# Kernel tuning notes

Measured on AMD Instinct MI355X. Metric: run time of the kernel, lower is better.

The kernel has to match this reference:

```python
import jax, jax.numpy as jnp
import numpy as np

D_MODEL = 768
D_STATE = 16
K_CONV = 4
BATCH = 2
SEQ = 2048


def setup_inputs() -> dict:
    key = jax.random.key(0)
    ks = jax.random.split(key, 16)
    dm, ds, K = D_MODEL, D_STATE, K_CONV
    s = 0.02
    inp = {
        "x": jax.random.normal(ks[0], (BATCH, SEQ, dm), dtype=jnp.float32),
        # linear weights stored (in, out); y = x @ W + b (equivalent to torch Linear)
        "Wi": jax.random.normal(ks[1], (dm, 2 * dm), dtype=jnp.float32) * s,
        "bi": jnp.zeros((2 * dm,), jnp.float32),
        "Wconv": jax.random.normal(ks[2], (dm, K), dtype=jnp.float32) * s,
        "bconv": jnp.zeros((dm,), jnp.float32),
        "Wdt": jax.random.normal(ks[3], (dm, dm), dtype=jnp.float32) * s,
        "bdt": jnp.zeros((dm,), jnp.float32),
        "WB": jax.random.normal(ks[4], (dm, dm * ds), dtype=jnp.float32) * s,
        "bB": jnp.zeros((dm * ds,), jnp.float32),
        "WC": jax.random.normal(ks[5], (dm, dm * ds), dtype=jnp.float32) * s,
        "bC": jnp.zeros((dm * ds,), jnp.float32),
        "A_log": jnp.zeros((dm, ds), jnp.float32),  # matches nn.Parameter(torch.zeros)
        "D": jnp.ones((dm,), jnp.float32),          # matches nn.Parameter(torch.ones)
        "Wo": jax.random.normal(ks[6], (dm, dm), dtype=jnp.float32) * s,
        "bo": jnp.zeros((dm,), jnp.float32),
    }
    return inp


def _forward(x, Wi, bi, Wconv, bconv, Wdt, bdt, WB, bB, WC, bC, A_log, D, Wo, bo):
    B, L, dm = x.shape
    ds = A_log.shape[1]
    K = Wconv.shape[1]

    uv = x @ Wi + bi                        # (B, L, 2*dm)
    u, v = uv[..., :dm], uv[..., dm:]

    # causal depthwise conv1d: torch pads K-1 both sides, keeps first L outputs
    u_pad = jnp.pad(u, ((0, 0), (K - 1, 0), (0, 0)))
    u_conv = bconv + sum(u_pad[:, k:k + L, :] * Wconv[:, k] for k in range(K))

    dt = jax.nn.softplus(u_conv @ Wdt + bdt)            # (B, L, dm)
    Bt = (u_conv @ WB + bB).reshape(B, L, dm, ds)       # (B, L, dm, ds)
    Ct = (u_conv @ WC + bC).reshape(B, L, dm, ds)
    A = -jnp.exp(A_log)                                  # (dm, ds)

    def step(s, inputs):
        dt_t, u_t, B_tt, C_tt = inputs                   # (B,dm), (B,dm), (B,dm,ds), (B,dm,ds)
        dt_e = dt_t[..., None]
        s = s * jnp.exp(dt_e * A) + dt_e * B_tt * u_t[..., None]
        y = jnp.sum(C_tt * s, axis=-1) + D * u_t         # (B, dm)
        return s, y

    s0 = jnp.zeros((B, dm, ds), x.dtype)
    xs = (dt.transpose(1, 0, 2), u_conv.transpose(1, 0, 2),
          Bt.transpose(1, 0, 2, 3), Ct.transpose(1, 0, 2, 3))
    _, ys = jax.lax.scan(step, s0, xs)                   # ys: (L, B, dm)
    y = ys.transpose(1, 0, 2)

    y = y * jax.nn.sigmoid(v)
    return y @ Wo + bo


def reference(x, Wi, bi, Wconv, bconv, Wdt, bdt, WB, bB, WC, bC, A_log, D, Wo, bo):
    return _forward(x, Wi, bi, Wconv, bconv, Wdt, bdt, WB, bB, WC, bC, A_log, D, Wo, bo)
```

## Files before the change

kernel.cpp:

```cpp
#include <hip/hip_runtime.h>

#define DM 768
#define DS 16
#define SEQ 2048
#define BATCH 2
#define MROWS (BATCH*SEQ)
#define N_UV (2*DM)
#define N_BC (DM*DS)
#define NGRP (BATCH*DM/4)
#define SUB 16

typedef _Float16 half8 __attribute__((ext_vector_type(8)));
typedef float floatx4 __attribute__((ext_vector_type(4)));

static __device__ __forceinline__ unsigned short f2h(float f) {
  _Float16 h = (_Float16)f;
  return __builtin_bit_cast(unsigned short, h);
}
static __device__ __forceinline__ float h2f(unsigned short u) {
  return (float)__builtin_bit_cast(_Float16, u);
}
static __device__ __forceinline__ float softplus_f(float x) {
  return (x > 20.f) ? x : log1pf(__expf(x));
}
static __device__ __forceinline__ void async_cp16(const unsigned short* g,
                                                  unsigned short* l) {
  __builtin_amdgcn_global_load_lds(
      (const __attribute__((address_space(1))) void*)g,
      (__attribute__((address_space(3))) void*)l, 16, 0, 0);
}

__global__ void convert_f2h(const float* __restrict__ in,
                            unsigned short* __restrict__ out, int n) {
  int i = (blockIdx.x * blockDim.x + threadIdx.x) * 4;
  if (i >= n) return;
  float4 f = *(const float4*)(in + i);
  ushort4 h;
  h.x = f2h(f.x); h.y = f2h(f.y); h.z = f2h(f.z); h.w = f2h(f.w);
  *(ushort4*)(out + i) = h;
}

__global__ void transpose_f2h(const float* __restrict__ W,
                              unsigned short* __restrict__ WT, int K, int N) {
  __shared__ float tile[32][33];
  int n0 = blockIdx.x * 32, k0 = blockIdx.y * 32;
  int tx = threadIdx.x, ty = threadIdx.y;
#pragma unroll
  for (int i = 0; i < 32; i += 8)
    tile[ty + i][tx] = W[(size_t)(k0 + ty + i) * N + (n0 + tx)];
  __syncthreads();
#pragma unroll
  for (int i = 0; i < 32; i += 8)
    WT[(size_t)(n0 + ty + i) * K + (k0 + tx)] = f2h(tile[tx][ty + i]);
}

template<int ACT, int OUTH>
__global__ __launch_bounds__(256)
void gemm_f16(const unsigned short* __restrict__ A,
              const unsigned short* __restrict__ BT,
              const float* __restrict__ bias,
              void* __restrict__ Cout,
              int M, int N, int K, int TCa, int bstride, int row0) {
  __shared__ __align__(16) unsigned short As[128 * 32];
  __shared__ __align__(16) unsigned short Bs[128 * 32];
  const int m0 = blockIdx.y * 128, n0 = blockIdx.x * 128;
  const int tid = threadIdx.x;
  const int lane = tid & 63, wave = tid >> 6;
  const int wm = (wave >> 1) * 64, wn = (wave & 1) * 64;
  const int l16 = lane & 15, quad = lane >> 4;
  const int sr = tid >> 2;
  const int sc = (tid & 3) * 8;

  floatx4 acc[4][4] = {};

  const int mA0 = m0 + sr, mA1 = m0 + sr + 64;
  const int gA0 = (mA0 / TCa) * bstride + row0 + (mA0 % TCa);
  const int gA1 = (mA1 / TCa) * bstride + row0 + (mA1 % TCa);
  const unsigned short* Arow0 = A + (size_t)gA0 * K + sc;
  const unsigned short* Arow1 = A + (size_t)gA1 * K + sc;
  const unsigned short* Brow0 = BT + (size_t)(n0 + sr) * K + sc;
  const unsigned short* Brow1 = BT + (size_t)(n0 + sr + 64) * K + sc;
  unsigned short* ldsA0 = As + (wave * 16) * 32;
  unsigned short* ldsA1 = As + (64 + wave * 16) * 32;
  unsigned short* ldsB0 = Bs + (wave * 16) * 32;
  unsigned short* ldsB1 = Bs + (64 + wave * 16) * 32;

  for (int k0 = 0; k0 < K; k0 += 32) {
    async_cp16(Arow0 + k0, ldsA0);
    async_cp16(Arow1 + k0, ldsA1);
    async_cp16(Brow0 + k0, ldsB0);
    async_cp16(Brow1 + k0, ldsB1);
    __syncthreads();
    half8 af[4], bf[4];
#pragma unroll
    for (int i = 0; i < 4; i++) {
      af[i] = __builtin_bit_cast(half8, *(const uint4*)&As[(wm + i * 16 + l16) * 32 + quad * 8]);
      bf[i] = __builtin_bit_cast(half8, *(const uint4*)&Bs[(wn + i * 16 + l16) * 32 + quad * 8]);
    }
#pragma unroll
    for (int mi = 0; mi < 4; mi++)
#pragma unroll
      for (int ni = 0; ni < 4; ni++)
        acc[mi][ni] = __builtin_amdgcn_mfma_f32_16x16x32_f16(af[mi], bf[ni], acc[mi][ni], 0, 0, 0);
    __syncthreads();
  }

#pragma unroll
  for (int ni = 0; ni < 4; ni++) {
    int col = n0 + wn + ni * 16 + l16;
    float bv = bias[col];
#pragma unroll
    for (int mi = 0; mi < 4; mi++) {
#pragma unroll
      for (int r = 0; r < 4; r++) {
        int row = m0 + wm + mi * 16 + quad * 4 + r;
        float v = acc[mi][ni][r] + bv;
        if (ACT == 1) v = softplus_f(v);
        if (OUTH) ((unsigned short*)Cout)[(size_t)row * N + col] = f2h(v);
        else      ((float*)Cout)[(size_t)row * N + col] = v;
      }
    }
  }
}

__global__ void dwconv(const unsigned short* __restrict__ uv,
                       const float* __restrict__ Wconv,
                       const float* __restrict__ bconv,
                       unsigned short* __restrict__ uc) {
  int idx = blockIdx.x * 256 + threadIdx.x;
  int c = idx % DM;
  int row = idx / DM;
  int t = row & (SEQ - 1);
  float acc = bconv[c];
  const float* w = Wconv + c * 4;
#pragma unroll
  for (int k = 0; k < 4; k++) {
    int tt = t - 3 + k;
    if (tt >= 0)
      acc += h2f(uv[(size_t)(row - 3 + k) * N_UV + c]) * w[k];
  }
  uc[(size_t)row * DM + c] = f2h(acc);
}

__global__ __launch_bounds__(64)
void scan_pass1(const unsigned short* __restrict__ dt,
                const unsigned short* __restrict__ uc,
                const unsigned short* __restrict__ Btc,
                const float* __restrict__ A_log,
                float* __restrict__ Ssub,
                float* __restrict__ Aexp,
                int ci, int TC) {
  const int TSUB = TC / SUB;
  int wid = blockIdx.x, sub = blockIdx.y;
  int b = wid / (DM / 4);
  int c0 = (wid % (DM / 4)) * 4;
  int lane = threadIdx.x;
  int c = c0 + (lane >> 4);
  float Acj = -__expf(A_log[c0 * DS + lane]);
  int col = c0 * DS + lane;
  size_t gbase = (size_t)b * SEQ + (size_t)ci * TC + (size_t)sub * TSUB;
  size_t lbase = (size_t)b * TC + (size_t)sub * TSUB;

  float s = 0.f, dsum = 0.f;
  float n_dt[8], n_u[8], n_B[8];
#pragma unroll
  for (int i = 0; i < 8; i++) {
    n_dt[i] = h2f(dt[(gbase + i) * DM + c]);
    n_u[i]  = h2f(uc[(gbase + i) * DM + c]);
    n_B[i]  = h2f(Btc[(lbase + i) * N_BC + col]);
  }
  for (int t0 = 0; t0 < TSUB; t0 += 8) {
    float c_dt[8], c_u[8], c_B[8];
#pragma unroll
    for (int i = 0; i < 8; i++) { c_dt[i] = n_dt[i]; c_u[i] = n_u[i]; c_B[i] = n_B[i]; }
    if (t0 + 8 < TSUB) {
#pragma unroll
      for (int i = 0; i < 8; i++) {
        size_t gr = gbase + t0 + 8 + i, lr = lbase + t0 + 8 + i;
        n_dt[i] = h2f(dt[gr * DM + c]);
        n_u[i]  = h2f(uc[gr * DM + c]);
        n_B[i]  = h2f(Btc[lr * N_BC + col]);
      }
    }
#pragma unroll
    for (int i = 0; i < 8; i++) {
      float dtc = c_dt[i];
      dsum += dtc;
      float a = __expf(dtc * Acj);
      s = fmaf(s, a, dtc * c_B[i] * c_u[i]);
    }
  }
  int idx = (sub * BATCH + b) * N_BC + col;
  Ssub[idx] = s;
  Aexp[idx] = __expf(Acj * dsum);
}

__global__ __launch_bounds__(64)
void scan_combine(const float* __restrict__ Ssub, const float* __restrict__ Aexp,
                  float* __restrict__ Sinit, float* __restrict__ s_state, int ci) {
  int wid = blockIdx.x;
  int b = wid / (DM / 4);
  int c0 = (wid % (DM / 4)) * 4;
  int col = c0 * DS + threadIdx.x;
  int sidx = b * N_BC + col;
  float s = (ci == 0) ? 0.f : s_state[sidx];
#pragma unroll
  for (int k = 0; k < SUB; k++) {
    int idx = (k * BATCH + b) * N_BC + col;
    Sinit[idx] = s;
    s = fmaf(s, Aexp[idx], Ssub[idx]);
  }
  s_state[sidx] = s;
}

__global__ __launch_bounds__(64)
void scan_pass2(const unsigned short* __restrict__ dt,
                const unsigned short* __restrict__ uc,
                const unsigned short* __restrict__ Btc,
                const unsigned short* __restrict__ Ctc,
                const unsigned short* __restrict__ uv,
                const float* __restrict__ A_log,
                const float* __restrict__ Dv,
                const float* __restrict__ Sinit,
                unsigned short* __restrict__ yg,
                int ci, int TC) {
  const int TSUB = TC / SUB;
  int wid = blockIdx.x, sub = blockIdx.y;
  int b = wid / (DM / 4);
  int c0 = (wid % (DM / 4)) * 4;
  int lane = threadIdx.x;
  int j = lane & 15;
  int c = c0 + (lane >> 4);
  float Acj = -__expf(A_log[c0 * DS + lane]);
  float Dc = Dv[c];
  int col = c0 * DS + lane;
  float s = Sinit[(sub * BATCH + b) * N_BC + col];
  size_t gbase = (size_t)b * SEQ + (size_t)ci * TC + (size_t)sub * TSUB;
  size_t lbase = (size_t)b * TC + (size_t)sub * TSUB;

  float n_dt[8], n_u[8], n_B[8], n_C[8], n_v[8];
#pragma unroll
  for (int i = 0; i < 8; i++) {
    size_t gr = gbase + i, lr = lbase + i;
    n_dt[i] = h2f(dt[gr * DM + c]);
    n_u[i]  = h2f(uc[gr * DM + c]);
    n_B[i]  = h2f(Btc[lr * N_BC + col]);
    n_C[i]  = h2f(Ctc[lr * N_BC + col]);
    n_v[i]  = h2f(uv[gr * N_UV + DM + c]);
  }
  for (int t0 = 0; t0 < TSUB; t0 += 8) {
    float c_dt[8], c_u[8], c_B[8], c_C[8], c_v[8];
#pragma unroll
    for (int i = 0; i < 8; i++) {
      c_dt[i] = n_dt[i]; c_u[i] = n_u[i]; c_B[i] = n_B[i];
      c_C[i] = n_C[i]; c_v[i] = n_v[i];
    }
    if (t0 + 8 < TSUB) {
#pragma unroll
      for (int i = 0; i < 8; i++) {
        size_t gr = gbase + t0 + 8 + i, lr = lbase + t0 + 8 + i;
        n_dt[i] = h2f(dt[gr * DM + c]);
        n_u[i]  = h2f(uc[gr * DM + c]);
        n_B[i]  = h2f(Btc[lr * N_BC + col]);
        n_C[i]  = h2f(Ctc[lr * N_BC + col]);
        n_v[i]  = h2f(uv[gr * N_UV + DM + c]);
      }
    }
#pragma unroll
    for (int i = 0; i < 8; i++) {
      float dtc = c_dt[i];
      float a = __expf(dtc * Acj);
      s = fmaf(s, a, dtc * c_B[i] * c_u[i]);
      float yt = c_C[i] * s;
      yt += __shfl_xor(yt, 8, 64);
      yt += __shfl_xor(yt, 4, 64);
      yt += __shfl_xor(yt, 2, 64);
      yt += __shfl_xor(yt, 1, 64);
      if (j == 0) {
        float y = yt + Dc * c_u[i];
        float g = 1.f / (1.f + __expf(-c_v[i]));
        yg[(gbase + t0 + i) * DM + c] = f2h(y * g);
      }
    }
  }
}

extern "C" void kernel_launch(void* const* d_in, const int* in_sizes, int n_in,
                              void* d_out, int out_size, void* d_ws, size_t ws_size,
                              hipStream_t stream) {
  const float* x     = (const float*)d_in[0];
  const float* Wi    = (const float*)d_in[1];
  const float* bi    = (const float*)d_in[2];
  const float* Wconv = (const float*)d_in[3];
  const float* bconv = (const float*)d_in[4];
  const float* Wdt   = (const float*)d_in[5];
  const float* bdt   = (const float*)d_in[6];
  const float* WB    = (const float*)d_in[7];
  const float* bB    = (const float*)d_in[8];
  const float* WC    = (const float*)d_in[9];
  const float* bC    = (const float*)d_in[10];
  const float* A_log = (const float*)d_in[11];
  const float* Dv    = (const float*)d_in[12];
  const float* Wo    = (const float*)d_in[13];
  const float* bo    = (const float*)d_in[14];
  float* out = (float*)d_out;
  (void)in_sizes; (void)n_in; (void)out_size;

  auto pad = [](size_t b) { return (b + 255) & ~(size_t)255; };

  const size_t sz_xb   = pad((size_t)MROWS * DM * 2);
  const size_t sz_WiT  = pad((size_t)N_UV * DM * 2);
  const size_t sz_WdtT = pad((size_t)DM * DM * 2);
  const size_t sz_WBT  = pad((size_t)N_BC * DM * 2);
  const size_t sz_WCT  = pad((size_t)N_BC * DM * 2);
  const size_t sz_WoT  = pad((size_t)DM * DM * 2);
  const size_t sz_uvb  = pad((size_t)MROWS * N_UV * 2);
  const size_t sz_ucb  = pad((size_t)MROWS * DM * 2);
  const size_t sz_dtb  = pad((size_t)MROWS * DM * 2);
  const size_t sz_st   = pad((size_t)BATCH * N_BC * 4);
  const size_t sz_sub  = pad((size_t)SUB * BATCH * N_BC * 4);
  const size_t fixed = sz_xb + sz_WiT + sz_WdtT + sz_WBT + sz_WCT + sz_WoT +
                       sz_uvb + sz_ucb + sz_dtb + sz_st + 3 * sz_sub;

  int NC = 16;
  for (int nc : {1, 2, 4, 8, 16}) {
    size_t need = fixed + 2 * pad((size_t)BATCH * (SEQ / nc) * N_BC * 2);
    if (need <= ws_size) { NC = nc; break; }
  }
  const int TC = SEQ / NC;
  const int MC = BATCH * TC;

  char* ws = (char*)d_ws;
  size_t off = 0;
  auto alloc = [&](size_t bytes) { char* p = ws + off; off += bytes; return p; };
  unsigned short* xb   = (unsigned short*)alloc(sz_xb);
  unsigned short* WiT  = (unsigned short*)alloc(sz_WiT);
  unsigned short* WdtT = (unsigned short*)alloc(sz_WdtT);
  unsigned short* WBT  = (unsigned short*)alloc(sz_WBT);
  unsigned short* WCT  = (unsigned short*)alloc(sz_WCT);
  unsigned short* WoT  = (unsigned short*)alloc(sz_WoT);
  unsigned short* uvb  = (unsigned short*)alloc(sz_uvb);
  unsigned short* ucb  = (unsigned short*)alloc(sz_ucb);
  unsigned short* dtb  = (unsigned short*)alloc(sz_dtb);
  float*          sst  = (float*)alloc(sz_st);
  float*          Ssub = (float*)alloc(sz_sub);
  float*          Aexp = (float*)alloc(sz_sub);
  float*          Sini = (float*)alloc(sz_sub);
  unsigned short* Btc  = (unsigned short*)alloc(pad((size_t)MC * N_BC * 2));
  unsigned short* Ctc  = (unsigned short*)alloc(pad((size_t)MC * N_BC * 2));
  unsigned short* ygb  = xb;

  convert_f2h<<<dim3(MROWS * DM / 1024), dim3(256), 0, stream>>>(x, xb, MROWS * DM);
  transpose_f2h<<<dim3(N_UV / 32, DM / 32), dim3(32, 8), 0, stream>>>(Wi, WiT, DM, N_UV);
  transpose_f2h<<<dim3(DM / 32, DM / 32), dim3(32, 8), 0, stream>>>(Wdt, WdtT, DM, DM);
  transpose_f2h<<<dim3(N_BC / 32, DM / 32), dim3(32, 8), 0, stream>>>(WB, WBT, DM, N_BC);
  transpose_f2h<<<dim3(N_BC / 32, DM / 32), dim3(32, 8), 0, stream>>>(WC, WCT, DM, N_BC);
  transpose_f2h<<<dim3(DM / 32, DM / 32), dim3(32, 8), 0, stream>>>(Wo, WoT, DM, DM);

  gemm_f16<0, 1><<<dim3(N_UV / 128, MROWS / 128), 256, 0, stream>>>(
      xb, WiT, bi, uvb, MROWS, N_UV, DM, MROWS, 0, 0);
  dwconv<<<dim3(MROWS * DM / 256), 256, 0, stream>>>(uvb, Wconv, bconv, ucb);
  gemm_f16<1, 1><<<dim3(DM / 128, MROWS / 128), 256, 0, stream>>>(
      ucb, WdtT, bdt, dtb, MROWS, DM, DM, MROWS, 0, 0);

  for (int ci = 0; ci < NC; ci++) {
    gemm_f16<0, 1><<<dim3(N_BC / 128, MC / 128), 256, 0, stream>>>(
        ucb, WBT, bB, Btc, MC, N_BC, DM, TC, SEQ, ci * TC);
    gemm_f16<0, 1><<<dim3(N_BC / 128, MC / 128), 256, 0, stream>>>(
        ucb, WCT, bC, Ctc, MC, N_BC, DM, TC, SEQ, ci * TC);
    scan_pass1<<<dim3(NGRP, SUB), 64, 0, stream>>>(dtb, ucb, Btc, A_log, Ssub, Aexp, ci, TC);
    scan_combine<<<dim3(NGRP), 64, 0, stream>>>(Ssub, Aexp, Sini, sst, ci);
    scan_pass2<<<dim3(NGRP, SUB), 64, 0, stream>>>(dtb, ucb, Btc, Ctc, uvb,
                                                   A_log, Dv, Sini, ygb, ci, TC);
  }

  gemm_f16<0, 0><<<dim3(DM / 128, MROWS / 128), 256, 0, stream>>>(
      ygb, WoT, bo, out, MROWS, DM, DM, MROWS, 0, 0);
}
```

Before: 655.8 us.

## Merge B/C GEMMs, swizzle GEMM LDS, vectorize dwconv, DPP reduce, adaptive scan splits

The B and C projection GEMMs now run as one launch, using blockIdx.z to pick weights, bias and output, so each chunk needs one fewer launch and the grid is larger. The GEMM applies an XOR swizzle to the LDS column chunks to cut bank conflicts on the fragment reads. The depthwise conv handles two channels per thread with paired half loads and stores. The scan's 16-lane reduction switches from shuffles to DPP row shifts, and the sub-chunk count is now set at runtime (up to 32) to expose more parallelism. Risks are the swizzle having to match exactly between the async copy writes and the fragment reads, and the DPP row masks being correct.

```diff
diff --git a/kernel.cpp b/kernel.cpp
--- a/kernel.cpp
+++ b/kernel.cpp
@@ -8,7 +8,7 @@
 #define N_UV (2*DM)
 #define N_BC (DM*DS)
 #define NGRP (BATCH*DM/4)
-#define SUB 16
+#define SUBMAX 32
 
 typedef _Float16 half8 __attribute__((ext_vector_type(8)));
 typedef float floatx4 __attribute__((ext_vector_type(4)));
@@ -28,6 +28,18 @@
   __builtin_amdgcn_global_load_lds(
       (const __attribute__((address_space(1))) void*)g,
       (__attribute__((address_space(3))) void*)l, 16, 0, 0);
+}
+static __device__ __forceinline__ float row_reduce16(float v) {
+  int x;
+  x = __builtin_amdgcn_update_dpp(0, __builtin_bit_cast(int, v), 0x128, 0xf, 0xf, true);
+  v += __builtin_bit_cast(float, x);
+  x = __builtin_amdgcn_update_dpp(0, __builtin_bit_cast(int, v), 0x124, 0xf, 0xf, true);
+  v += __builtin_bit_cast(float, x);
+  x = __builtin_amdgcn_update_dpp(0, __builtin_bit_cast(int, v), 0x122, 0xf, 0xf, true);
+  v += __builtin_bit_cast(float, x);
+  x = __builtin_amdgcn_update_dpp(0, __builtin_bit_cast(int, v), 0x121, 0xf, 0xf, true);
+  v += __builtin_bit_cast(float, x);
+  return v;
 }
 
 __global__ void convert_f2h(const float* __restrict__ in,
@@ -57,10 +69,16 @@
 template<int ACT, int OUTH>
 __global__ __launch_bounds__(256)
 void gemm_f16(const unsigned short* __restrict__ A,
-              const unsigned short* __restrict__ BT,
-              const float* __restrict__ bias,
-              void* __restrict__ Cout,
+              const unsigned short* __restrict__ BT0,
+              const unsigned short* __restrict__ BT1,
+              const float* __restrict__ bias0,
+              const float* __restrict__ bias1,
+              void* __restrict__ Cout0,
+              void* __restrict__ Cout1,
               int M, int N, int K, int TCa, int bstride, int row0) {
+  const unsigned short* BT = blockIdx.z ? BT1 : BT0;
+  const float* bias = blockIdx.z ? bias1 : bias0;
+  void* Cout = blockIdx.z ? Cout1 : Cout0;
   __shared__ __align__(16) unsigned short As[128 * 32];
   __shared__ __align__(16) unsigned short Bs[128 * 32];
   const int m0 = blockIdx.y * 128, n0 = blockIdx.x * 128;
@@ -69,7 +87,8 @@
   const int wm = (wave >> 1) * 64, wn = (wave & 1) * 64;
   const int l16 = lane & 15, quad = lane >> 4;
   const int sr = tid >> 2;
-  const int sc = (tid & 3) * 8;
+  const int sc = (((tid & 3) ^ ((tid >> 3) & 3)) ) * 8;
+  const int pch = (quad ^ ((l16 >> 1) & 3)) * 8;
 
   floatx4 acc[4][4] = {};
 
@@ -94,8 +113,8 @@
     half8 af[4], bf[4];
 #pragma unroll
     for (int i = 0; i < 4; i++) {
-      af[i] = __builtin_bit_cast(half8, *(const uint4*)&As[(wm + i * 16 + l16) * 32 + quad * 8]);
-      bf[i] = __builtin_bit_cast(half8, *(const uint4*)&Bs[(wn + i * 16 + l16) * 32 + quad * 8]);
+      af[i] = __builtin_bit_cast(half8, *(const uint4*)&As[(wm + i * 16 + l16) * 32 + pch]);
+      bf[i] = __builtin_bit_cast(half8, *(const uint4*)&Bs[(wn + i * 16 + l16) * 32 + pch]);
     }
 #pragma unroll
     for (int mi = 0; mi < 4; mi++)
@@ -128,18 +147,23 @@
                        const float* __restrict__ bconv,
                        unsigned short* __restrict__ uc) {
   int idx = blockIdx.x * 256 + threadIdx.x;
-  int c = idx % DM;
-  int row = idx / DM;
+  int c = (idx % (DM / 2)) * 2;
+  int row = idx / (DM / 2);
   int t = row & (SEQ - 1);
-  float acc = bconv[c];
-  const float* w = Wconv + c * 4;
+  float a0 = bconv[c], a1 = bconv[c + 1];
+  const float* w0 = Wconv + c * 4;
+  const float* w1 = Wconv + (c + 1) * 4;
 #pragma unroll
   for (int k = 0; k < 4; k++) {
     int tt = t - 3 + k;
-    if (tt >= 0)
-      acc += h2f(uv[(size_t)(row - 3 + k) * N_UV + c]) * w[k];
-  }
-  uc[(size_t)row * DM + c] = f2h(acc);
+    if (tt >= 0) {
+      ushort2 u2 = *(const ushort2*)&uv[(size_t)(row - 3 + k) * N_UV + c];
+      a0 += h2f(u2.x) * w0[k];
+      a1 += h2f(u2.y) * w1[k];
+    }
+  }
+  ushort2 o; o.x = f2h(a0); o.y = f2h(a1);
+  *(ushort2*)&uc[(size_t)row * DM + c] = o;
 }
 
 __global__ __launch_bounds__(64)
@@ -149,8 +173,8 @@
                 const float* __restrict__ A_log,
                 float* __restrict__ Ssub,
                 float* __restrict__ Aexp,
-                int ci, int TC) {
-  const int TSUB = TC / SUB;
+                int ci, int TC, int SUBn) {
+  const int TSUB = TC / SUBn;
   int wid = blockIdx.x, sub = blockIdx.y;
   int b = wid / (DM / 4);
   int c0 = (wid % (DM / 4)) * 4;
@@ -197,15 +221,15 @@
 
 __global__ __launch_bounds__(64)
 void scan_combine(const float* __restrict__ Ssub, const float* __restrict__ Aexp,
-                  float* __restrict__ Sinit, float* __restrict__ s_state, int ci) {
+                  float* __restrict__ Sinit, float* __restrict__ s_state,
+                  int ci, int SUBn) {
   int wid = blockIdx.x;
   int b = wid / (DM / 4);
   int c0 = (wid % (DM / 4)) * 4;
   int col = c0 * DS + threadIdx.x;
   int sidx = b * N_BC + col;
   float s = (ci == 0) ? 0.f : s_state[sidx];
-#pragma unroll
-  for (int k = 0; k < SUB; k++) {
+  for (int k = 0; k < SUBn; k++) {
     int idx = (k * BATCH + b) * N_BC + col;
     Sinit[idx] = s;
     s = fmaf(s, Aexp[idx], Ssub[idx]);
@@ -223,8 +247,8 @@
                 const float* __restrict__ Dv,
                 const float* __restrict__ Sinit,
                 unsigned short* __restrict__ yg,
-                int ci, int TC) {
-  const int TSUB = TC / SUB;
+                int ci, int TC, int SUBn) {
+  const int TSUB = TC / SUBn;
   int wid = blockIdx.x, sub = blockIdx.y;
   int b = wid / (DM / 4);
   int c0 = (wid % (DM / 4)) * 4;
@@ -271,11 +295,7 @@
       float dtc = c_dt[i];
       float a = __expf(dtc * Acj);
       s = fmaf(s, a, dtc * c_B[i] * c_u[i]);
-      float yt = c_C[i] * s;
-      yt += __shfl_xor(yt, 8, 64);
-      yt += __shfl_xor(yt, 4, 64);
-      yt += __shfl_xor(yt, 2, 64);
-      yt += __shfl_xor(yt, 1, 64);
+      float yt = row_reduce16(c_C[i] * s);
       if (j == 0) {
         float y = yt + Dc * c_u[i];
         float g = 1.f / (1.f + __expf(-c_v[i]));
@@ -318,7 +338,7 @@
   const size_t sz_ucb  = pad((size_t)MROWS * DM * 2);
   const size_t sz_dtb  = pad((size_t)MROWS * DM * 2);
   const size_t sz_st   = pad((size_t)BATCH * N_BC * 4);
-  const size_t sz_sub  = pad((size_t)SUB * BATCH * N_BC * 4);
+  const size_t sz_sub  = pad((size_t)SUBMAX * BATCH * N_BC * 4);
   const size_t fixed = sz_xb + sz_WiT + sz_WdtT + sz_WBT + sz_WCT + sz_WoT +
                        sz_uvb + sz_ucb + sz_dtb + sz_st + 3 * sz_sub;
 
@@ -329,6 +349,7 @@
   }
   const int TC = SEQ / NC;
   const int MC = BATCH * TC;
+  const int SUBn = (TC / 8 < SUBMAX) ? (TC / 8) : SUBMAX;
 
   char* ws = (char*)d_ws;
   size_t off = 0;
@@ -357,23 +378,21 @@
   transpose_f2h<<<dim3(N_BC / 32, DM / 32), dim3(32, 8), 0, stream>>>(WC, WCT, DM, N_BC);
   transpose_f2h<<<dim3(DM / 32, DM / 32), dim3(32, 8), 0, stream>>>(Wo, WoT, DM, DM);
 
-  gemm_f16<0, 1><<<dim3(N_UV / 128, MROWS / 128), 256, 0, stream>>>(
-      xb, WiT, bi, uvb, MROWS, N_UV, DM, MROWS, 0, 0);
-  dwconv<<<dim3(MROWS * DM / 256), 256, 0, stream>>>(uvb, Wconv, bconv, ucb);
-  gemm_f16<1, 1><<<dim3(DM / 128, MROWS / 128), 256, 0, stream>>>(
-      ucb, WdtT, bdt, dtb, MROWS, DM, DM, MROWS, 0, 0);
+  gemm_f16<0, 1><<<dim3(N_UV / 128, MROWS / 128, 1), 256, 0, stream>>>(
+      xb, WiT, WiT, bi, bi, uvb, uvb, MROWS, N_UV, DM, MROWS, 0, 0);
+  dwconv<<<dim3(MROWS * DM / 512), 256, 0, stream>>>(uvb, Wconv, bconv, ucb);
+  gemm_f16<1, 1><<<dim3(DM / 128, MROWS / 128, 1), 256, 0, stream>>>(
+      ucb, WdtT, WdtT, bdt, bdt, dtb, dtb, MROWS, DM, DM, MROWS, 0, 0);
 
   for (int ci = 0; ci < NC; ci++) {
-    gemm_f16<0, 1><<<dim3(N_BC / 128, MC / 128), 256, 0, stream>>>(
-        ucb, WBT, bB, Btc, MC, N_BC, DM, TC, SEQ, ci * TC);
-    gemm_f16<0, 1><<<dim3(N_BC / 128, MC / 128), 256, 0, stream>>>(
-        ucb, WCT, bC, Ctc, MC, N_BC, DM, TC, SEQ, ci * TC);
-    scan_pass1<<<dim3(NGRP, SUB), 64, 0, stream>>>(dtb, ucb, Btc, A_log, Ssub, Aexp, ci, TC);
-    scan_combine<<<dim3(NGRP), 64, 0, stream>>>(Ssub, Aexp, Sini, sst, ci);
-    scan_pass2<<<dim3(NGRP, SUB), 64, 0, stream>>>(dtb, ucb, Btc, Ctc, uvb,
-                                                   A_log, Dv, Sini, ygb, ci, TC);
-  }
-
-  gemm_f16<0, 0><<<dim3(DM / 128, MROWS / 128), 256, 0, stream>>>(
-      ygb, WoT, bo, out, MROWS, DM, DM, MROWS, 0, 0);
-}
+    gemm_f16<0, 1><<<dim3(N_BC / 128, MC / 128, 2), 256, 0, stream>>>(
+        ucb, WBT, WCT, bB, bC, Btc, Ctc, MC, N_BC, DM, TC, SEQ, ci * TC);
+    scan_pass1<<<dim3(NGRP, SUBn), 64, 0, stream>>>(dtb, ucb, Btc, A_log, Ssub, Aexp, ci, TC, SUBn);
+    scan_combine<<<dim3(NGRP), 64, 0, stream>>>(Ssub, Aexp, Sini, sst, ci, SUBn);
+    scan_pass2<<<dim3(NGRP, SUBn), 64, 0, stream>>>(dtb, ucb, Btc, Ctc, uvb,
+                                                    A_log, Dv, Sini, ygb, ci, TC, SUBn);
+  }
+
+  gemm_f16<0, 0><<<dim3(DM / 128, MROWS / 128, 1), 256, 0, stream>>>(
+      ygb, WoT, WoT, bo, bo, out, out, MROWS, DM, DM, MROWS, 0, 0);
+}
```

After: 626.8 us. 1.05x faster.
